# Kernel optimization log

Hardware: AMD Instinct MI355X
Metric: run time of the kernel (lower is better)

Reference implementation:

```python
import jax, jax.numpy as jnp
import numpy as np

NUM_BOND_TYPE = 6
NUM_BOND_DIRECTION = 3
N_NODES = 20000
N_EDGES = 320000
HIDDEN = 256
OUT = 256
N_MASK = 2000


def setup_inputs() -> dict:
    key = jax.random.key(0)
    ks = jax.random.split(key, 12)
    x = jax.random.normal(ks[0], (N_NODES, HIDDEN), dtype=jnp.float32)
    edge_index = jax.random.randint(ks[1], (2, N_EDGES), 0, N_NODES, dtype=jnp.int64)
    edge_attr = jax.random.randint(ks[2], (N_EDGES, 2), 0, 3, dtype=jnp.int64)
    mask_node_indices = jax.random.randint(ks[3], (N_MASK,), 0, N_NODES, dtype=jnp.int64)
    # parameters (torch Linear convention: y = x @ W.T + b)
    def xavier(k, shape):
        fan_in, fan_out = shape[1], shape[0]
        lim = float(np.sqrt(6.0 / (fan_in + fan_out)))
        return jax.random.uniform(k, shape, jnp.float32, -lim, lim)
    prelu_a = jnp.asarray(0.25, dtype=jnp.float32)  # torch PReLU default
    W_enc = xavier(ks[4], (HIDDEN, HIDDEN))          # enc_to_dec, no bias
    E1 = xavier(ks[5], (NUM_BOND_TYPE, HIDDEN))
    E2 = xavier(ks[6], (NUM_BOND_DIRECTION, HIDDEN))
    W1 = xavier(ks[7], (2 * HIDDEN, HIDDEN))
    b1 = jnp.zeros((2 * HIDDEN,), jnp.float32)
    W2 = xavier(ks[8], (OUT, 2 * HIDDEN))
    b2 = jnp.zeros((OUT,), jnp.float32)
    return {"x": x, "edge_index": edge_index, "edge_attr": edge_attr,
            "mask_node_indices": mask_node_indices, "prelu_a": prelu_a,
            "W_enc": W_enc, "E1": E1, "E2": E2,
            "W1": W1, "b1": b1, "W2": W2, "b2": b2}


def reference(x, edge_index, edge_attr, mask_node_indices, prelu_a,
              W_enc, E1, E2, W1, b1, W2, b2):
    N = x.shape[0]
    # PReLU -> enc_to_dec linear (no bias) -> zero masked rows
    x = jnp.where(x >= 0, x, prelu_a * x)
    x = x @ W_enc.T
    x = x.at[mask_node_indices].set(0.0)
    # add self loops: (i,i) edges with attr (4, 0)
    loop = jnp.arange(N, dtype=edge_index.dtype)
    ei = jnp.concatenate([edge_index, jnp.stack([loop, loop])], axis=1)  # [2, E+N]
    loop_attr = jnp.concatenate(
        [jnp.full((N, 1), 4, edge_attr.dtype), jnp.zeros((N, 1), edge_attr.dtype)], axis=1)
    ea = jnp.concatenate([edge_attr, loop_attr], axis=0)                 # [E+N, 2]
    edge_emb = E1[ea[:, 0]] + E2[ea[:, 1]]                               # [E+N, D]
    src, dst = ei[0], ei[1]                                              # j -> i
    msg = x[src] + edge_emb                                              # [E+N, D]
    aggr = jax.ops.segment_sum(msg, dst, num_segments=N)                 # [N, D]
    # GIN MLP: Linear -> ReLU -> Linear
    h = jax.nn.relu(aggr @ W1.T + b1)
    return h @ W2.T + b2
```

## Files before the change

kernel.cpp:

```cpp
#include <hip/hip_runtime.h>

#define HIDDEN 256
#define CAP 64

typedef _Float16 h4_t __attribute__((ext_vector_type(4)));
typedef _Float16 h8_t __attribute__((ext_vector_type(8)));
typedef float    f4_t __attribute__((ext_vector_type(4)));

typedef const __attribute__((address_space(1))) void* gbl_ptr_t;
typedef __attribute__((address_space(3))) void*       lds_ptr_t;

__global__ __launch_bounds__(256) void k_prep(
        const float* __restrict__ x, _Float16* __restrict__ xh,
        const float* __restrict__ prelu_a, int M, int Mpad, int nb_x,
        const int* __restrict__ ei, const int* __restrict__ ea, int E,
        int* __restrict__ cnt, int* __restrict__ csr, int nb_fill,
        const float* __restrict__ W_enc, const float* __restrict__ W1,
        const float* __restrict__ W2, _Float16* __restrict__ Whenc,
        _Float16* __restrict__ Wh1, _Float16* __restrict__ Wh2, int nb_w,
        const int* __restrict__ mask, unsigned char* __restrict__ flags, int NM) {
    int b = blockIdx.x;
    int t = threadIdx.x;
    if (b < nb_x) {
        int base = (b * 256 + t) * 4;
        if (base >= Mpad * HIDDEN) return;
        int row = base >> 8;
        h4_t o;
        if (row < M) {
            float pa = *prelu_a;
            f4_t v = *(const f4_t*)(x + base);
            o.x = (_Float16)(v.x >= 0.f ? v.x : pa * v.x);
            o.y = (_Float16)(v.y >= 0.f ? v.y : pa * v.y);
            o.z = (_Float16)(v.z >= 0.f ? v.z : pa * v.z);
            o.w = (_Float16)(v.w >= 0.f ? v.w : pa * v.w);
        } else {
            o = (h4_t)(_Float16)0.f;
        }
        *(h4_t*)(xh + base) = o;
        return;
    }
    b -= nb_x;
    if (b < nb_fill) {
        int e = b * 256 + t;
        if (e >= E) return;
        int src = ei[e];
        int dst = ei[E + e];
        int combo = ea[2 * e] * 3 + ea[2 * e + 1];
        int slot = atomicAdd(&cnt[dst], 1);
        csr[dst * CAP + slot] = src | (combo << 16);
        return;
    }
    b -= nb_fill;
    if (b < nb_w) {
        const int n0 = HIDDEN * HIDDEN, n1 = 2 * HIDDEN * HIDDEN, n2 = HIDDEN * 2 * HIDDEN;
        int base = (b * 256 + t) * 4;
        const float* s; _Float16* d; int off;
        if (base < n0) { s = W_enc; d = Whenc; off = base; }
        else if (base < n0 + n1) { s = W1; d = Wh1; off = base - n0; }
        else if (base < n0 + n1 + n2) { s = W2; d = Wh2; off = base - n0 - n1; }
        else return;
        f4_t v = *(const f4_t*)(s + off);
        h4_t o; o.x = (_Float16)v.x; o.y = (_Float16)v.y;
        o.z = (_Float16)v.z; o.w = (_Float16)v.w;
        *(h4_t*)(d + off) = o;
        return;
    }
    b -= nb_w;
    {
        int i = b * 256 + t;
        if (i < NM) flags[mask[i]] = 1;
    }
}

__global__ __launch_bounds__(256) void k_aggregate(
        const _Float16* __restrict__ xe,
        const float* __restrict__ E1, const float* __restrict__ E2,
        const int* __restrict__ cnt, const int* __restrict__ csr,
        _Float16* __restrict__ aggr, int N, int Mpad) {
    __shared__ __align__(16) _Float16 e12h[18 * HIDDEN];
    int t = threadIdx.x;
    for (int idx = t; idx < 18 * 64; idx += 256) {
        int combo = idx >> 6, c4 = (idx & 63) * 4;
        int a1 = combo / 3, a2 = combo - a1 * 3;
        f4_t v1 = *(const f4_t*)(E1 + a1 * HIDDEN + c4);
        f4_t v2 = *(const f4_t*)(E2 + a2 * HIDDEN + c4);
        h4_t o;
        o.x = (_Float16)(v1.x + v2.x); o.y = (_Float16)(v1.y + v2.y);
        o.z = (_Float16)(v1.z + v2.z); o.w = (_Float16)(v1.w + v2.w);
        *(h4_t*)(e12h + combo * HIDDEN + c4) = o;
    }
    __syncthreads();
    int node = blockIdx.x * 4 + (t >> 6);
    if (node >= Mpad) return;
    int c0 = (t & 63) * 4;
    if (node >= N) {
        *(h4_t*)(aggr + (size_t)node * HIDDEN + c0) = (h4_t)(_Float16)0.f;
        return;
    }

    h4_t hs = *(const h4_t*)(xe + (size_t)node * HIDDEN + c0);
    h4_t se = *(const h4_t*)(e12h + 12 * HIDDEN + c0);
    f4_t acc;
    acc.x = (float)hs.x + (float)se.x; acc.y = (float)hs.y + (float)se.y;
    acc.z = (float)hs.z + (float)se.z; acc.w = (float)hs.w + (float)se.w;

    const int* lst = csr + (size_t)node * CAP;
    int deg = cnt[node];
    int e = 0;
    for (; e + 3 < deg; e += 4) {
        int p0 = lst[e], p1 = lst[e + 1], p2 = lst[e + 2], p3 = lst[e + 3];
        h4_t h0 = *(const h4_t*)(xe + (size_t)(p0 & 0xFFFF) * HIDDEN + c0);
        h4_t h1 = *(const h4_t*)(xe + (size_t)(p1 & 0xFFFF) * HIDDEN + c0);
        h4_t h2 = *(const h4_t*)(xe + (size_t)(p2 & 0xFFFF) * HIDDEN + c0);
        h4_t h3 = *(const h4_t*)(xe + (size_t)(p3 & 0xFFFF) * HIDDEN + c0);
        h4_t q0 = *(const h4_t*)(e12h + (p0 >> 16) * HIDDEN + c0);
        h4_t q1 = *(const h4_t*)(e12h + (p1 >> 16) * HIDDEN + c0);
        h4_t q2 = *(const h4_t*)(e12h + (p2 >> 16) * HIDDEN + c0);
        h4_t q3 = *(const h4_t*)(e12h + (p3 >> 16) * HIDDEN + c0);
        h4_t s01 = (h0 + q0) + (h1 + q1);
        h4_t s23 = (h2 + q2) + (h3 + q3);
        acc.x += (float)s01.x + (float)s23.x;
        acc.y += (float)s01.y + (float)s23.y;
        acc.z += (float)s01.z + (float)s23.z;
        acc.w += (float)s01.w + (float)s23.w;
    }
    for (; e < deg; ++e) {
        int p0 = lst[e];
        h4_t h0 = *(const h4_t*)(xe + (size_t)(p0 & 0xFFFF) * HIDDEN + c0);
        h4_t q0 = *(const h4_t*)(e12h + (p0 >> 16) * HIDDEN + c0);
        h4_t s0 = h0 + q0;
        acc.x += (float)s0.x; acc.y += (float)s0.y;
        acc.z += (float)s0.z; acc.w += (float)s0.w;
    }
    h4_t o;
    o.x = (_Float16)acc.x; o.y = (_Float16)acc.y;
    o.z = (_Float16)acc.z; o.w = (_Float16)acc.w;
    *(h4_t*)(aggr + (size_t)node * HIDDEN + c0) = o;
}

template <bool RELU, bool HAS_BIAS, bool OUT_F16, bool MASK>
__global__ __launch_bounds__(128) void k_mfma_gemm(
        const _Float16* __restrict__ A, const _Float16* __restrict__ B,
        const float* __restrict__ bias, void* __restrict__ Cout,
        const unsigned char* __restrict__ flags,
        int Mstore, int N, int K) {
    __shared__ __align__(16) _Float16 As[2][128 * 32];
    __shared__ __align__(16) _Float16 Bs[2][64 * 32];
    int t = threadIdx.x;
    int w = t >> 6, L = t & 63;
    int m0 = blockIdx.x * 128, n0 = blockIdx.y * 64;
    int wm = w * 64;
    int lrow = L & 15, lk = (L >> 4) * 8;

    f4_t acc[4][4] = {};

    auto stage = [&](int k0, int b) {
#pragma unroll
        for (int i = 0; i < 4; ++i) {
            int c = t + 128 * i;
            __builtin_amdgcn_global_load_lds(
                (gbl_ptr_t)(A + (size_t)(m0 + (c >> 2)) * K + k0 + (c & 3) * 8),
                (lds_ptr_t)(&As[b][c * 8]), 16, 0, 0);
        }
#pragma unroll
        for (int i = 0; i < 2; ++i) {
            int c = t + 128 * i;
            __builtin_amdgcn_global_load_lds(
                (gbl_ptr_t)(B + (size_t)(n0 + (c >> 2)) * K + k0 + (c & 3) * 8),
                (lds_ptr_t)(&Bs[b][c * 8]), 16, 0, 0);
        }
    };

    stage(0, 0);
    int nstep = K >> 5;
    for (int s = 0; s < nstep; ++s) {
        int b = s & 1;
        __syncthreads();
        if (s + 1 < nstep) stage((s + 1) << 5, b ^ 1);
        h8_t af[4], bf[4];
#pragma unroll
        for (int i = 0; i < 4; ++i)
            af[i] = *(const h8_t*)&As[b][(wm + i * 16 + lrow) * 32 + lk];
#pragma unroll
        for (int j = 0; j < 4; ++j)
            bf[j] = *(const h8_t*)&Bs[b][(j * 16 + lrow) * 32 + lk];
#pragma unroll
        for (int i = 0; i < 4; ++i)
#pragma unroll
            for (int j = 0; j < 4; ++j)
                acc[i][j] = __builtin_amdgcn_mfma_f32_16x16x32_f16(af[i], bf[j], acc[i][j], 0, 0, 0);
    }

    int lcol = L & 15, lr4 = (L >> 4) * 4;
    float zmul[4][4];
#pragma unroll
    for (int i = 0; i < 4; ++i)
#pragma unroll
        for (int r = 0; r < 4; ++r) {
            int row = m0 + wm + i * 16 + lr4 + r;
            zmul[i][r] = (MASK && flags[row]) ? 0.f : 1.f;
        }
#pragma unroll
    for (int j = 0; j < 4; ++j) {
        int col = n0 + j * 16 + lcol;
        float bv = HAS_BIAS ? bias[col] : 0.f;
#pragma unroll
        for (int i = 0; i < 4; ++i) {
#pragma unroll
            for (int r = 0; r < 4; ++r) {
                int row = m0 + wm + i * 16 + lr4 + r;
                float v = (acc[i][j][r] + bv) * zmul[i][r];
                if (RELU) v = v > 0.f ? v : 0.f;
                if (OUT_F16) {
                    ((_Float16*)Cout)[(size_t)row * N + col] = (_Float16)v;
                } else {
                    if (row < Mstore) ((float*)Cout)[(size_t)row * N + col] = v;
                }
            }
        }
    }
}

extern "C" void kernel_launch(void* const* d_in, const int* in_sizes, int n_in,
                              void* d_out, int out_size, void* d_ws, size_t ws_size,
                              hipStream_t stream) {
    const float* x       = (const float*)d_in[0];
    const int*   ei      = (const int*)d_in[1];
    const int*   ea      = (const int*)d_in[2];
    const int*   mask    = (const int*)d_in[3];
    const float* prelu_a = (const float*)d_in[4];
    const float* W_enc   = (const float*)d_in[5];
    const float* E1      = (const float*)d_in[6];
    const float* E2      = (const float*)d_in[7];
    const float* W1      = (const float*)d_in[8];
    const float* b1      = (const float*)d_in[9];
    const float* W2      = (const float*)d_in[10];
    const float* b2      = (const float*)d_in[11];
    float*       out     = (float*)d_out;

    int N  = in_sizes[0] / HIDDEN;
    int E  = in_sizes[1] / 2;
    int NM = in_sizes[3];
    int Mpad = ((N + 127) / 128) * 128;

    char* ws = (char*)d_ws;
    size_t off = 0;
    _Float16* xh    = (_Float16*)(ws + off); off += (size_t)Mpad * HIDDEN * 2;
    _Float16* XEh   = (_Float16*)(ws + off); off += (size_t)Mpad * HIDDEN * 2;
    _Float16* AGh   = (_Float16*)(ws + off); off += (size_t)Mpad * HIDDEN * 2;
    _Float16* Hh    = (_Float16*)(ws + off); off += (size_t)Mpad * 2 * HIDDEN * 2;
    _Float16* Whenc = (_Float16*)(ws + off); off += (size_t)HIDDEN * HIDDEN * 2;
    _Float16* Wh1   = (_Float16*)(ws + off); off += (size_t)2 * HIDDEN * HIDDEN * 2;
    _Float16* Wh2   = (_Float16*)(ws + off); off += (size_t)HIDDEN * 2 * HIDDEN * 2;
    int* cnt        = (int*)(ws + off);      off += (size_t)N * 4;
    unsigned char* flags = (unsigned char*)(ws + off); off += (size_t)Mpad;
    off = (off + 15) & ~(size_t)15;
    int* csr        = (int*)(ws + off);      off += (size_t)N * CAP * 4;

    hipMemsetAsync(cnt, 0, (size_t)N * 4 + (size_t)Mpad, stream);

    int nb_x    = (Mpad * HIDDEN / 4 + 255) / 256;
    int nb_fill = (E + 255) / 256;
    int wtot4   = (HIDDEN * HIDDEN + 2 * HIDDEN * HIDDEN + HIDDEN * 2 * HIDDEN) / 4;
    int nb_w    = (wtot4 + 255) / 256;
    int nb_m    = (NM + 255) / 256;
    k_prep<<<nb_x + nb_fill + nb_w + nb_m, 256, 0, stream>>>(
        x, xh, prelu_a, N, Mpad, nb_x,
        ei, ea, E, cnt, csr, nb_fill,
        W_enc, W1, W2, Whenc, Wh1, Wh2, nb_w,
        mask, flags, NM);

    dim3 g1(Mpad / 128, HIDDEN / 64);
    k_mfma_gemm<false, false, true, true><<<g1, 128, 0, stream>>>(
        xh, Whenc, nullptr, XEh, flags, N, HIDDEN, HIDDEN);

    k_aggregate<<<(Mpad + 3) / 4, 256, 0, stream>>>(XEh, E1, E2, cnt, csr, AGh, N, Mpad);

    dim3 g2(Mpad / 128, 2 * HIDDEN / 64);
    k_mfma_gemm<true, true, true, false><<<g2, 128, 0, stream>>>(
        AGh, Wh1, b1, Hh, nullptr, N, 2 * HIDDEN, HIDDEN);

    dim3 g3(Mpad / 128, HIDDEN / 64);
    k_mfma_gemm<false, true, false, false><<<g3, 128, 0, stream>>>(
        Hh, Wh2, b2, out, nullptr, N, HIDDEN, 2 * HIDDEN);
}
```

Before: 194.9 us.

## Fuse GIN MLP into one kernel, direct-load GEMMs, shuffle-broadcast CSR in aggregation

Fuses the two MLP GEMMs into one kernel that keeps the 64x512 ReLU hidden tile in LDS, so the fp16 hidden buffer is never written to or read from global memory. The encoder GEMM is replaced by a version that loads fragments straight from global memory into registers, without LDS staging or double buffering. The aggregation now loads each node's neighbour list once per wavefront and broadcasts entries with shuffles, with 8-way unrolled gathers. It also clamps the CSR slot count to CAP; direct global fragment loads may lose coalescing, and the MLP kernel uses about 65KB of LDS, which limits occupancy.

```diff
diff --git a/kernel.cpp b/kernel.cpp
--- a/kernel.cpp
+++ b/kernel.cpp
@@ -7,8 +7,10 @@
 typedef _Float16 h8_t __attribute__((ext_vector_type(8)));
 typedef float    f4_t __attribute__((ext_vector_type(4)));
 
-typedef const __attribute__((address_space(1))) void* gbl_ptr_t;
-typedef __attribute__((address_space(3))) void*       lds_ptr_t;
+__device__ inline f4_t cvt4(h4_t h) {
+    f4_t o; o.x = (float)h.x; o.y = (float)h.y; o.z = (float)h.z; o.w = (float)h.w;
+    return o;
+}
 
 __global__ __launch_bounds__(256) void k_prep(
         const float* __restrict__ x, _Float16* __restrict__ xh,
@@ -47,7 +49,7 @@
         int dst = ei[E + e];
         int combo = ea[2 * e] * 3 + ea[2 * e + 1];
         int slot = atomicAdd(&cnt[dst], 1);
-        csr[dst * CAP + slot] = src | (combo << 16);
+        if (slot < CAP) csr[dst * CAP + slot] = src | (combo << 16);
         return;
     }
     b -= nb_fill;
@@ -92,45 +94,44 @@
     __syncthreads();
     int node = blockIdx.x * 4 + (t >> 6);
     if (node >= Mpad) return;
-    int c0 = (t & 63) * 4;
+    int lane = t & 63;
+    int c0 = lane * 4;
     if (node >= N) {
         *(h4_t*)(aggr + (size_t)node * HIDDEN + c0) = (h4_t)(_Float16)0.f;
         return;
     }
+    int deg = cnt[node];
+    if (deg > CAP) deg = CAP;
+    const int* lst = csr + (size_t)node * CAP;
+    int pv = (lane < deg) ? lst[lane] : 0;
 
     h4_t hs = *(const h4_t*)(xe + (size_t)node * HIDDEN + c0);
     h4_t se = *(const h4_t*)(e12h + 12 * HIDDEN + c0);
-    f4_t acc;
-    acc.x = (float)hs.x + (float)se.x; acc.y = (float)hs.y + (float)se.y;
-    acc.z = (float)hs.z + (float)se.z; acc.w = (float)hs.w + (float)se.w;
-
-    const int* lst = csr + (size_t)node * CAP;
-    int deg = cnt[node];
+    f4_t acc = cvt4(hs) + cvt4(se);
+
     int e = 0;
-    for (; e + 3 < deg; e += 4) {
-        int p0 = lst[e], p1 = lst[e + 1], p2 = lst[e + 2], p3 = lst[e + 3];
-        h4_t h0 = *(const h4_t*)(xe + (size_t)(p0 & 0xFFFF) * HIDDEN + c0);
-        h4_t h1 = *(const h4_t*)(xe + (size_t)(p1 & 0xFFFF) * HIDDEN + c0);
-        h4_t h2 = *(const h4_t*)(xe + (size_t)(p2 & 0xFFFF) * HIDDEN + c0);
-        h4_t h3 = *(const h4_t*)(xe + (size_t)(p3 & 0xFFFF) * HIDDEN + c0);
-        h4_t q0 = *(const h4_t*)(e12h + (p0 >> 16) * HIDDEN + c0);
-        h4_t q1 = *(const h4_t*)(e12h + (p1 >> 16) * HIDDEN + c0);
-        h4_t q2 = *(const h4_t*)(e12h + (p2 >> 16) * HIDDEN + c0);
-        h4_t q3 = *(const h4_t*)(e12h + (p3 >> 16) * HIDDEN + c0);
-        h4_t s01 = (h0 + q0) + (h1 + q1);
-        h4_t s23 = (h2 + q2) + (h3 + q3);
-        acc.x += (float)s01.x + (float)s23.x;
-        acc.y += (float)s01.y + (float)s23.y;
-        acc.z += (float)s01.z + (float)s23.z;
-        acc.w += (float)s01.w + (float)s23.w;
+    for (; e + 7 < deg; e += 8) {
+        int p[8]; h4_t hv[8], qv[8];
+#pragma unroll
+        for (int j = 0; j < 8; ++j) p[j] = __shfl(pv, e + j, 64);
+#pragma unroll
+        for (int j = 0; j < 8; ++j)
+            hv[j] = *(const h4_t*)(xe + (size_t)(p[j] & 0xFFFF) * HIDDEN + c0);
+#pragma unroll
+        for (int j = 0; j < 8; ++j)
+            qv[j] = *(const h4_t*)(e12h + (p[j] >> 16) * HIDDEN + c0);
+        h4_t s0 = (hv[0] + qv[0]) + (hv[1] + qv[1]);
+        h4_t s1 = (hv[2] + qv[2]) + (hv[3] + qv[3]);
+        h4_t s2 = (hv[4] + qv[4]) + (hv[5] + qv[5]);
+        h4_t s3 = (hv[6] + qv[6]) + (hv[7] + qv[7]);
+        acc += cvt4(s0) + cvt4(s1);
+        acc += cvt4(s2) + cvt4(s3);
     }
     for (; e < deg; ++e) {
-        int p0 = lst[e];
-        h4_t h0 = *(const h4_t*)(xe + (size_t)(p0 & 0xFFFF) * HIDDEN + c0);
-        h4_t q0 = *(const h4_t*)(e12h + (p0 >> 16) * HIDDEN + c0);
-        h4_t s0 = h0 + q0;
-        acc.x += (float)s0.x; acc.y += (float)s0.y;
-        acc.z += (float)s0.z; acc.w += (float)s0.w;
+        int p = __shfl(pv, e, 64);
+        h4_t h = *(const h4_t*)(xe + (size_t)(p & 0xFFFF) * HIDDEN + c0);
+        h4_t q = *(const h4_t*)(e12h + (p >> 16) * HIDDEN + c0);
+        acc += cvt4(h + q);
     }
     h4_t o;
     o.x = (_Float16)acc.x; o.y = (_Float16)acc.y;
@@ -138,52 +139,25 @@
     *(h4_t*)(aggr + (size_t)node * HIDDEN + c0) = o;
 }
 
-template <bool RELU, bool HAS_BIAS, bool OUT_F16, bool MASK>
-__global__ __launch_bounds__(128) void k_mfma_gemm(
+template <int K, bool MASK>
+__global__ __launch_bounds__(256) void k_gemm_direct(
         const _Float16* __restrict__ A, const _Float16* __restrict__ B,
-        const float* __restrict__ bias, void* __restrict__ Cout,
-        const unsigned char* __restrict__ flags,
-        int Mstore, int N, int K) {
-    __shared__ __align__(16) _Float16 As[2][128 * 32];
-    __shared__ __align__(16) _Float16 Bs[2][64 * 32];
-    int t = threadIdx.x;
-    int w = t >> 6, L = t & 63;
-    int m0 = blockIdx.x * 128, n0 = blockIdx.y * 64;
-    int wm = w * 64;
-    int lrow = L & 15, lk = (L >> 4) * 8;
+        _Float16* __restrict__ C, const unsigned char* __restrict__ flags, int N) {
+    int t = threadIdx.x, w = t >> 6, L = t & 63;
+    int m0 = blockIdx.x * 128 + (w >> 1) * 64;
+    int n0 = blockIdx.y * 128 + (w & 1) * 64;
+    int lr = L & 15, lk = (L >> 4) * 8;
 
     f4_t acc[4][4] = {};
-
-    auto stage = [&](int k0, int b) {
-#pragma unroll
-        for (int i = 0; i < 4; ++i) {
-            int c = t + 128 * i;
-            __builtin_amdgcn_global_load_lds(
-                (gbl_ptr_t)(A + (size_t)(m0 + (c >> 2)) * K + k0 + (c & 3) * 8),
-                (lds_ptr_t)(&As[b][c * 8]), 16, 0, 0);
-        }
-#pragma unroll
-        for (int i = 0; i < 2; ++i) {
-            int c = t + 128 * i;
-            __builtin_amdgcn_global_load_lds(
-                (gbl_ptr_t)(B + (size_t)(n0 + (c >> 2)) * K + k0 + (c & 3) * 8),
-                (lds_ptr_t)(&Bs[b][c * 8]), 16, 0, 0);
-        }
-    };
-
-    stage(0, 0);
-    int nstep = K >> 5;
-    for (int s = 0; s < nstep; ++s) {
-        int b = s & 1;
-        __syncthreads();
-        if (s + 1 < nstep) stage((s + 1) << 5, b ^ 1);
+    const _Float16* Ab = A + (size_t)(m0 + lr) * K + lk;
+    const _Float16* Bb = B + (size_t)(n0 + lr) * K + lk;
+#pragma unroll
+    for (int s = 0; s < K / 32; ++s) {
         h8_t af[4], bf[4];
 #pragma unroll
-        for (int i = 0; i < 4; ++i)
-            af[i] = *(const h8_t*)&As[b][(wm + i * 16 + lrow) * 32 + lk];
-#pragma unroll
-        for (int j = 0; j < 4; ++j)
-            bf[j] = *(const h8_t*)&Bs[b][(j * 16 + lrow) * 32 + lk];
+        for (int i = 0; i < 4; ++i) af[i] = *(const h8_t*)(Ab + i * 16 * K + s * 32);
+#pragma unroll
+        for (int j = 0; j < 4; ++j) bf[j] = *(const h8_t*)(Bb + j * 16 * K + s * 32);
 #pragma unroll
         for (int i = 0; i < 4; ++i)
 #pragma unroll
@@ -191,32 +165,91 @@
                 acc[i][j] = __builtin_amdgcn_mfma_f32_16x16x32_f16(af[i], bf[j], acc[i][j], 0, 0, 0);
     }
 
-    int lcol = L & 15, lr4 = (L >> 4) * 4;
-    float zmul[4][4];
+    int lr4 = (L >> 4) * 4;
 #pragma unroll
     for (int i = 0; i < 4; ++i)
 #pragma unroll
         for (int r = 0; r < 4; ++r) {
-            int row = m0 + wm + i * 16 + lr4 + r;
-            zmul[i][r] = (MASK && flags[row]) ? 0.f : 1.f;
-        }
-#pragma unroll
-    for (int j = 0; j < 4; ++j) {
-        int col = n0 + j * 16 + lcol;
-        float bv = HAS_BIAS ? bias[col] : 0.f;
-#pragma unroll
-        for (int i = 0; i < 4; ++i) {
-#pragma unroll
-            for (int r = 0; r < 4; ++r) {
-                int row = m0 + wm + i * 16 + lr4 + r;
-                float v = (acc[i][j][r] + bv) * zmul[i][r];
-                if (RELU) v = v > 0.f ? v : 0.f;
-                if (OUT_F16) {
-                    ((_Float16*)Cout)[(size_t)row * N + col] = (_Float16)v;
-                } else {
-                    if (row < Mstore) ((float*)Cout)[(size_t)row * N + col] = v;
+            int row = m0 + i * 16 + lr4 + r;
+            float zm = (MASK && flags[row]) ? 0.f : 1.f;
+#pragma unroll
+            for (int j = 0; j < 4; ++j) {
+                int col = n0 + j * 16 + lr;
+                C[(size_t)row * N + col] = (_Float16)(acc[i][j][r] * zm);
+            }
+        }
+}
+
+__global__ __launch_bounds__(256) void k_mlp(
+        const _Float16* __restrict__ AG, const _Float16* __restrict__ W1h,
+        const float* __restrict__ b1, const _Float16* __restrict__ W2h,
+        const float* __restrict__ b2, float* __restrict__ out, int Mstore) {
+    __shared__ __align__(16) _Float16 Hs[64 * 520];
+    int t = threadIdx.x, w = t >> 6, L = t & 63;
+    int m0 = blockIdx.x * 64;
+    int lr = L & 15, lk = (L >> 4) * 8, lr4 = (L >> 4) * 4;
+
+    {
+        f4_t acc[4][8] = {};
+        const _Float16* Ab = AG + (size_t)(m0 + lr) * 256 + lk;
+        const _Float16* Bb = W1h + (size_t)(w * 128 + lr) * 256 + lk;
+#pragma unroll
+        for (int s = 0; s < 8; ++s) {
+            h8_t af[4];
+#pragma unroll
+            for (int i = 0; i < 4; ++i) af[i] = *(const h8_t*)(Ab + i * 16 * 256 + s * 32);
+            h8_t bf[8];
+#pragma unroll
+            for (int j = 0; j < 8; ++j) bf[j] = *(const h8_t*)(Bb + j * 16 * 256 + s * 32);
+#pragma unroll
+            for (int i = 0; i < 4; ++i)
+#pragma unroll
+                for (int j = 0; j < 8; ++j)
+                    acc[i][j] = __builtin_amdgcn_mfma_f32_16x16x32_f16(af[i], bf[j], acc[i][j], 0, 0, 0);
+        }
+#pragma unroll
+        for (int j = 0; j < 8; ++j) {
+            int n = w * 128 + j * 16 + lr;
+            float bv = b1[n];
+#pragma unroll
+            for (int i = 0; i < 4; ++i)
+#pragma unroll
+                for (int r = 0; r < 4; ++r) {
+                    float v = acc[i][j][r] + bv;
+                    v = v > 0.f ? v : 0.f;
+                    Hs[(i * 16 + lr4 + r) * 520 + n] = (_Float16)v;
                 }
-            }
+        }
+    }
+    __syncthreads();
+    {
+        f4_t acc[4][4] = {};
+        const _Float16* Bb = W2h + (size_t)(w * 64 + lr) * 512 + lk;
+#pragma unroll
+        for (int s = 0; s < 16; ++s) {
+            h8_t af[4], bf[4];
+#pragma unroll
+            for (int i = 0; i < 4; ++i)
+                af[i] = *(const h8_t*)&Hs[(i * 16 + lr) * 520 + s * 32 + lk];
+#pragma unroll
+            for (int j = 0; j < 4; ++j) bf[j] = *(const h8_t*)(Bb + j * 16 * 512 + s * 32);
+#pragma unroll
+            for (int i = 0; i < 4; ++i)
+#pragma unroll
+                for (int j = 0; j < 4; ++j)
+                    acc[i][j] = __builtin_amdgcn_mfma_f32_16x16x32_f16(af[i], bf[j], acc[i][j], 0, 0, 0);
+        }
+#pragma unroll
+        for (int j = 0; j < 4; ++j) {
+            int col = w * 64 + j * 16 + lr;
+            float bv = b2[col];
+#pragma unroll
+            for (int i = 0; i < 4; ++i)
+#pragma unroll
+                for (int r = 0; r < 4; ++r) {
+                    int row = m0 + i * 16 + lr4 + r;
+                    if (row < Mstore) out[(size_t)row * 256 + col] = acc[i][j][r] + bv;
+                }
         }
     }
 }
@@ -248,7 +281,6 @@
     _Float16* xh    = (_Float16*)(ws + off); off += (size_t)Mpad * HIDDEN * 2;
     _Float16* XEh   = (_Float16*)(ws + off); off += (size_t)Mpad * HIDDEN * 2;
     _Float16* AGh   = (_Float16*)(ws + off); off += (size_t)Mpad * HIDDEN * 2;
-    _Float16* Hh    = (_Float16*)(ws + off); off += (size_t)Mpad * 2 * HIDDEN * 2;
     _Float16* Whenc = (_Float16*)(ws + off); off += (size_t)HIDDEN * HIDDEN * 2;
     _Float16* Wh1   = (_Float16*)(ws + off); off += (size_t)2 * HIDDEN * HIDDEN * 2;
     _Float16* Wh2   = (_Float16*)(ws + off); off += (size_t)HIDDEN * 2 * HIDDEN * 2;
@@ -270,17 +302,10 @@
         W_enc, W1, W2, Whenc, Wh1, Wh2, nb_w,
         mask, flags, NM);
 
-    dim3 g1(Mpad / 128, HIDDEN / 64);
-    k_mfma_gemm<false, false, true, true><<<g1, 128, 0, stream>>>(
-        xh, Whenc, nullptr, XEh, flags, N, HIDDEN, HIDDEN);
+    dim3 g1(Mpad / 128, HIDDEN / 128);
+    k_gemm_direct<HIDDEN, true><<<g1, 256, 0, stream>>>(xh, Whenc, XEh, flags, HIDDEN);
 
     k_aggregate<<<(Mpad + 3) / 4, 256, 0, stream>>>(XEh, E1, E2, cnt, csr, AGh, N, Mpad);
 
-    dim3 g2(Mpad / 128, 2 * HIDDEN / 64);
-    k_mfma_gemm<true, true, true, false><<<g2, 128, 0, stream>>>(
-        AGh, Wh1, b1, Hh, nullptr, N, 2 * HIDDEN, HIDDEN);
-
-    dim3 g3(Mpad / 128, HIDDEN / 64);
-    k_mfma_gemm<false, true, false, false><<<g3, 128, 0, stream>>>(
-        Hh, Wh2, b2, out, nullptr, N, HIDDEN, 2 * HIDDEN);
-}
+    k_mlp<<<Mpad / 64, 256, 0, stream>>>(AGh, Wh1, b1, Wh2, b2, out, N);
+}
```

Result: slower. 215.9 us (+10.8%).
